# Optimization experiments

Measured on AMD Instinct MI355X. Metric: run time of the kernel, lower is better.

## Reference

```python
import jax, jax.numpy as jnp
import numpy as np

K, PAD, POOL = 3, 1, 2

def _conv_block(x, w, b):
    # x: [B,C,H,W]; w: [O, C*K*K] (Linear weight, feature order (C,kh,kw)); b: [O]
    O = w.shape[0]
    C = x.shape[1]
    ker = w.reshape(O, C, K, K)  # OIHW, matches torch unfold+linear ordering
    y = jax.lax.conv_general_dilated(
        x, ker, window_strides=(1, 1), padding=[(PAD, PAD), (PAD, PAD)],
        dimension_numbers=("NCHW", "OIHW", "NCHW"))
    y = y + b[None, :, None, None]
    y = jax.nn.relu(y)
    # non-overlapping max pool, drops remainder like torch unfold (sizes divisible here)
    y = jax.lax.reduce_window(y, -jnp.inf, jax.lax.max,
                              (1, 1, POOL, POOL), (1, 1, POOL, POOL), "VALID")
    return y

def setup_inputs() -> dict:
    key = jax.random.key(0)
    ks = jax.random.split(key, 9)
    B, Cin, H = 64, 3, 128
    C1, C2, FC, NCLS = 64, 128, 256, 1000
    flat = C2 * (H // 4) * (H // 4)  # 128*32*32 = 131072
    s = 0.05
    return {
        "x": jax.random.normal(ks[0], (B, Cin, H, H), jnp.float32),
        "conv1_w": jax.random.normal(ks[1], (C1, Cin * K * K), jnp.float32) * s,
        "conv1_b": jax.random.normal(ks[2], (C1,), jnp.float32) * s,
        "conv2_w": jax.random.normal(ks[3], (C2, C1 * K * K), jnp.float32) * s,
        "conv2_b": jax.random.normal(ks[4], (C2,), jnp.float32) * s,
        "fc1_w": jax.random.normal(ks[5], (FC, flat), jnp.float32) * 0.005,
        "fc1_b": jax.random.normal(ks[6], (FC,), jnp.float32) * s,
        "fc2_w": jax.random.normal(ks[7], (NCLS, FC), jnp.float32) * s,
        "fc2_b": jax.random.normal(ks[8], (NCLS,), jnp.float32) * s,
    }

def reference(x, conv1_w, conv1_b, conv2_w, conv2_b, fc1_w, fc1_b, fc2_w, fc2_b):
    h = _conv_block(x, conv1_w, conv1_b)      # [B,64,64,64]
    h = _conv_block(h, conv2_w, conv2_b)      # [B,128,32,32]
    h = h.reshape(h.shape[0], -1)             # NCHW flatten, same as torch .view
    h = jax.nn.relu(h @ fc1_w.T + fc1_b)
    return h @ fc2_w.T + fc2_b                # [B,1000]
```

## Files before the change

kernel.cpp:

```cpp
#include <hip/hip_runtime.h>
#include <hip/hip_bf16.h>

typedef __attribute__((ext_vector_type(8))) short short8;
typedef __attribute__((ext_vector_type(4))) float f32x4;

#define KFC   131072
#define NCLS  1000

__device__ __forceinline__ unsigned short f2bf(float f) {
  union { float f; unsigned u; } v; v.f = f;
  unsigned r = v.u + 0x7FFFu + ((v.u >> 16) & 1u);
  return (unsigned short)(r >> 16);
}

__device__ __forceinline__ unsigned pk2bf(float a, float b) {
  __hip_bfloat162 h = __float22bfloat162_rn(float2{a, b});
  union { __hip_bfloat162 h; unsigned u; } c; c.h = h;
  return c.u;
}

__global__ __launch_bounds__(256) void prep_w1(
    const float* __restrict__ w1, short* __restrict__ Bp1) {
  int i = blockIdx.x * 256 + threadIdx.x;
  int o = i >> 5, k = i & 31;
  Bp1[i] = (k < 27) ? (short)f2bf(w1[o * 27 + k]) : (short)0;
}

__global__ __launch_bounds__(256) void conv1_mfma(
    const float* __restrict__ x, const short* __restrict__ Bp1,
    const float* __restrict__ b1, unsigned short* __restrict__ y) {
  __shared__ unsigned short tile[1152];
  const int t = threadIdx.x;
  const int blk = blockIdx.x;
  const int tx = blk & 7, ty = (blk >> 3) & 7, b = blk >> 6;
  const int w = t >> 6, lane = t & 63;
  const int l15 = lane & 15, lg = lane >> 4;

  const int ih0 = ty * 16 - 1, iw0 = tx * 16 - 1;
  for (int i = t; i < 1152; i += 256) {
    unsigned short v = 0;
    if (i < 1080) {
      int ci = i / 360, rem = i - ci * 360;
      int tr = rem / 20, tc = rem - tr * 20;
      int ih = ih0 + tr, iw = iw0 + tc;
      if (tc < 18 && (unsigned)ih < 128u && (unsigned)iw < 128u)
        v = f2bf(x[(b * 3 + ci) * 16384 + (ih << 7) + iw]);
    }
    tile[i] = v;
  }

  short8 bf[4];
#pragma unroll
  for (int n = 0; n < 4; ++n)
    bf[n] = *(const short8*)(Bp1 + ((n * 16 + l15) << 5) + (lg << 3));

  int soff[8];
#pragma unroll
  for (int j = 0; j < 8; ++j) {
    int k = lg * 8 + j;
    if (k < 27) {
      int ci = k / 9, rem = k - ci * 9;
      int r = rem / 3, s = rem - r * 3;
      soff[j] = ci * 360 + r * 20 + s + l15 + w * 80;
    } else {
      soff[j] = 1080;
    }
  }
  __syncthreads();

  f32x4 acc[4][4];
#pragma unroll
  for (int m = 0; m < 4; ++m)
#pragma unroll
    for (int n = 0; n < 4; ++n) acc[m][n] = (f32x4){0.f, 0.f, 0.f, 0.f};

#pragma unroll
  for (int m = 0; m < 4; ++m) {
    union { short8 s; unsigned short u[8]; } af;
#pragma unroll
    for (int j = 0; j < 8; ++j) af.u[j] = tile[soff[j] + m * 20];
#pragma unroll
    for (int n = 0; n < 4; ++n)
      acc[m][n] = __builtin_amdgcn_mfma_f32_16x16x32_bf16(af.s, bf[n], acc[m][n], 0, 0, 0);
  }

#pragma unroll
  for (int n = 0; n < 4; ++n) {
    const int o = n * 16 + l15;
    const float bias = b1[o];
#pragma unroll
    for (int q = 0; q < 2; ++q) {
      const int pr = ty * 8 + w * 2 + q;
      float v0 = fmaxf(fmaxf(acc[2 * q][n][0], acc[2 * q][n][1]),
                       fmaxf(acc[2 * q + 1][n][0], acc[2 * q + 1][n][1]));
      float v1 = fmaxf(fmaxf(acc[2 * q][n][2], acc[2 * q][n][3]),
                       fmaxf(acc[2 * q + 1][n][2], acc[2 * q + 1][n][3]));
      v0 = fmaxf(v0 + bias, 0.f);
      v1 = fmaxf(v1 + bias, 0.f);
      const int pc = tx * 8 + lg * 2;
      unsigned short* dst = y + ((((size_t)b << 6) + pr) << 12) + ((size_t)pc << 6) + o;
      dst[0]  = f2bf(v0);
      dst[64] = f2bf(v1);
    }
  }
}

__global__ __launch_bounds__(256) void prep_w2(
    const float* __restrict__ w2, short* __restrict__ Bp) {
  int i = blockIdx.x * 256 + threadIdx.x;
  int c = i & 31, o = (i >> 5) & 127, pp = i >> 12;
  int cg = pp / 9, pos = pp - cg * 9;
  Bp[i] = (short)f2bf(w2[o * 576 + (cg * 32 + c) * 9 + pos]);
}

__global__ __launch_bounds__(256) void conv2_mfma(
    const short* __restrict__ yin, const short* __restrict__ Bp,
    const float* __restrict__ b2, unsigned int* __restrict__ A32) {
  __shared__ short tile[180 * 36];
  const int t = threadIdx.x;
  const int blk = blockIdx.x;
  const int tx = blk & 3, ty = (blk >> 2) & 7, b = blk >> 5;
  const int w = t >> 6, lane = t & 63;
  const int l15 = lane & 15, lg = lane >> 4;

  f32x4 acc[8][2];
#pragma unroll
  for (int m = 0; m < 8; ++m)
#pragma unroll
    for (int n = 0; n < 2; ++n) acc[m][n] = (f32x4){0.f, 0.f, 0.f, 0.f};

  const int ih0 = ty * 8 - 1, iw0 = tx * 16 - 1;
  const int abase = l15 * 36 + lg * 8;

#pragma unroll
  for (int cg = 0; cg < 2; ++cg) {
    __syncthreads();
    for (int i = t; i < 180 * 4; i += 256) {
      int p = i >> 2, q = i & 3;
      int sy = p / 18, sx = p - sy * 18;
      int ih = ih0 + sy, iw = iw0 + sx;
      short8 v = (short8){0, 0, 0, 0, 0, 0, 0, 0};
      if (((unsigned)ih < 64u) && ((unsigned)iw < 64u))
        v = *(const short8*)(yin + ((((size_t)b << 6) + ih) << 12) + ((size_t)iw << 6) + cg * 32 + q * 8);
      *(short8*)&tile[p * 36 + q * 8] = v;
    }
    __syncthreads();

    short8 afb[2][4];
    short8 bfb[2][2];

#pragma unroll
    for (int n = 0; n < 2; ++n)
      bfb[0][n] = *(const short8*)(Bp + ((((cg * 9 + 0) << 7) + (w * 2 + n) * 16 + l15) << 5) + (lg << 3));
#pragma unroll
    for (int m = 0; m < 4; ++m)
      afb[0][m] = *(const short8*)&tile[m * 648 + abase];

#pragma unroll
    for (int s = 0; s < 18; ++s) {
      const int pos = s >> 1, half = s & 1;
      if (s < 17) {
        const int ns = s + 1, npos = ns >> 1, nhalf = ns & 1;
        if (nhalf == 0) {
#pragma unroll
          for (int n = 0; n < 2; ++n)
            bfb[npos & 1][n] = *(const short8*)(Bp + ((((cg * 9 + npos) << 7) + (w * 2 + n) * 16 + l15) << 5) + (lg << 3));
        }
        const int nkh = npos / 3, nkw = npos - nkh * 3;
#pragma unroll
        for (int m = 0; m < 4; ++m)
          afb[ns & 1][m] = *(const short8*)&tile[(nhalf * 4 + m + nkh) * 648 + nkw * 36 + abase];
      }
#pragma unroll
      for (int n = 0; n < 2; ++n)
#pragma unroll
        for (int m = 0; m < 4; ++m)
          acc[half * 4 + m][n] = __builtin_amdgcn_mfma_f32_16x16x32_bf16(
              afb[s & 1][m], bfb[pos & 1][n], acc[half * 4 + m][n], 0, 0, 0);
    }
  }

  const size_t bbase = ((size_t)b << 16);
#pragma unroll
  for (int n = 0; n < 2; ++n) {
    const int o = (w * 2 + n) * 16 + l15;
    const float bias = b2[o];
#pragma unroll
    for (int mp = 0; mp < 4; ++mp) {
      const int prow = ty * 4 + mp;
      float v0 = fmaxf(fmaxf(acc[2 * mp][n][0], acc[2 * mp][n][1]),
                       fmaxf(acc[2 * mp + 1][n][0], acc[2 * mp + 1][n][1]));
      float v1 = fmaxf(fmaxf(acc[2 * mp][n][2], acc[2 * mp][n][3]),
                       fmaxf(acc[2 * mp + 1][n][2], acc[2 * mp + 1][n][3]));
      v0 = fmaxf(v0 + bias, 0.f);
      v1 = fmaxf(v1 + bias, 0.f);
      unsigned pk = (unsigned)f2bf(v0) | ((unsigned)f2bf(v1) << 16);
      A32[bbase + (size_t)o * 512 + prow * 16 + tx * 4 + lg] = pk;
    }
  }
}

__global__ __launch_bounds__(256) void fc1_mfma(
    const unsigned short* __restrict__ A, const float* __restrict__ W,
    float* __restrict__ P) {
  __shared__ short Al[64][520];
  const int t = threadIdx.x;
  const int blk = blockIdx.x;
  const int kc = blk >> 1, nt = blk & 1;
  const int wn = t >> 6, lane = t & 63;
  const int l15 = lane & 15, lg = lane >> 4;

  {
    const int row = t >> 2, q = t & 3;
    const unsigned short* asrc = A + (size_t)row * KFC + kc * 512 + q * 128;
    short8 ar[16];
#pragma unroll
    for (int i = 0; i < 16; ++i) ar[i] = *(const short8*)(asrc + i * 8);
#pragma unroll
    for (int i = 0; i < 16; ++i) *(short8*)&Al[row][q * 128 + i * 8] = ar[i];
  }
  __syncthreads();

  f32x4 acc[4][2];
#pragma unroll
  for (int m = 0; m < 4; ++m)
#pragma unroll
    for (int n = 0; n < 2; ++n) acc[m][n] = (f32x4){0.f, 0.f, 0.f, 0.f};

  const float* wrow[2];
#pragma unroll
  for (int n = 0; n < 2; ++n)
    wrow[n] = W + (size_t)(nt * 128 + wn * 32 + n * 16 + l15) * KFC + kc * 512 + lg * 8;

#pragma unroll
  for (int ks = 0; ks < 16; ++ks) {
    short8 bf[2];
#pragma unroll
    for (int n = 0; n < 2; ++n) {
      f32x4 u = *(const f32x4*)(wrow[n] + ks * 32);
      f32x4 v = *(const f32x4*)(wrow[n] + ks * 32 + 4);
      union { short8 s; unsigned u32[4]; } pk;
      pk.u32[0] = pk2bf(u[0], u[1]);
      pk.u32[1] = pk2bf(u[2], u[3]);
      pk.u32[2] = pk2bf(v[0], v[1]);
      pk.u32[3] = pk2bf(v[2], v[3]);
      bf[n] = pk.s;
    }
    short8 af[4];
#pragma unroll
    for (int m = 0; m < 4; ++m)
      af[m] = *(const short8*)&Al[m * 16 + l15][ks * 32 + lg * 8];
#pragma unroll
    for (int n = 0; n < 2; ++n)
#pragma unroll
      for (int m = 0; m < 4; ++m)
        acc[m][n] = __builtin_amdgcn_mfma_f32_16x16x32_bf16(af[m], bf[n], acc[m][n], 0, 0, 0);
  }

  float* dst = P + (size_t)kc * 16384;
#pragma unroll
  for (int m = 0; m < 4; ++m)
#pragma unroll
    for (int n = 0; n < 2; ++n)
#pragma unroll
      for (int j = 0; j < 4; ++j) {
        int brow = m * 16 + lg * 4 + j;
        int o = nt * 128 + wn * 32 + n * 16 + l15;
        dst[brow * 256 + o] = acc[m][n][j];
      }
}

__global__ __launch_bounds__(256) void fc1_reduce_kernel(
    const float* __restrict__ P, const float* __restrict__ fb1,
    float* __restrict__ Y) {
  __shared__ float red[4][64];
  const int t = threadIdx.x;
  const int iq = t & 63, pg = t >> 6;
  const int gidx = blockIdx.x * 64 + iq;
  const float* p0 = P + (size_t)(pg * 64) * 16384 + gidx;
  float s0 = 0, s1 = 0, s2 = 0, s3 = 0;
  for (int p = 0; p < 64; p += 4) {
    s0 += p0[(size_t)(p + 0) * 16384];
    s1 += p0[(size_t)(p + 1) * 16384];
    s2 += p0[(size_t)(p + 2) * 16384];
    s3 += p0[(size_t)(p + 3) * 16384];
  }
  red[pg][iq] = (s0 + s1) + (s2 + s3);
  __syncthreads();
  if (pg == 0) {
    float tot = (red[0][iq] + red[1][iq]) + (red[2][iq] + red[3][iq]);
    Y[gidx] = fmaxf(tot + fb1[gidx & 255], 0.f);
  }
}

__global__ __launch_bounds__(256) void fc2_kernel(
    const float* __restrict__ Y, const float* __restrict__ W2,
    const float* __restrict__ b2, float* __restrict__ out) {
  int tid = blockIdx.x * 256 + threadIdx.x;
  if (tid >= 64 * NCLS) return;
  int b = tid / NCLS, n = tid - b * NCLS;
  const float4* yv = (const float4*)(Y + b * 256);
  const float4* wv = (const float4*)(W2 + n * 256);
  float acc = 0.f;
#pragma unroll 8
  for (int f = 0; f < 64; ++f) {
    float4 a = yv[f], w = wv[f];
    acc += a.x * w.x + a.y * w.y + a.z * w.z + a.w * w.w;
  }
  out[tid] = acc + b2[n];
}

extern "C" void kernel_launch(void* const* d_in, const int* in_sizes, int n_in,
                              void* d_out, int out_size, void* d_ws, size_t ws_size,
                              hipStream_t stream) {
  const float* x   = (const float*)d_in[0];
  const float* w1  = (const float*)d_in[1];
  const float* b1  = (const float*)d_in[2];
  const float* w2  = (const float*)d_in[3];
  const float* b2  = (const float*)d_in[4];
  const float* fw1 = (const float*)d_in[5];
  const float* fb1 = (const float*)d_in[6];
  const float* fw2 = (const float*)d_in[7];
  const float* fb2 = (const float*)d_in[8];
  float* out = (float*)d_out;

  unsigned short* Y1 = (unsigned short*)d_ws;
  unsigned short* A16 = Y1 + 16777216;
  short* Bp = (short*)(A16 + 8388608);
  short* Bp1 = Bp + 73728;
  float* P  = (float*)(Bp1 + 2048);
  float* Yf = P + 4194304;

  prep_w2<<<288, 256, 0, stream>>>(w2, Bp);
  prep_w1<<<8, 256, 0, stream>>>(w1, Bp1);
  conv1_mfma<<<4096, 256, 0, stream>>>(x, Bp1, b1, Y1);
  conv2_mfma<<<2048, 256, 0, stream>>>((const short*)Y1, Bp, b2, (unsigned int*)A16);
  fc1_mfma<<<512, 256, 0, stream>>>(A16, fw1, P);
  fc1_reduce_kernel<<<256, 256, 0, stream>>>(P, fb1, Yf);
  fc2_kernel<<<250, 256, 0, stream>>>(Yf, fw2, fb2, out);
}
```

Measured before the change: 116.5 us.

## Switch conv2 to 32x32x16 MFMA with full-channel LDS tile

Conv2 now uses 32x32x16 bf16 MFMA instructions instead of 16x16x32. Each wave computes 32 output channels across 4 pairs of output rows. The LDS tile holds all 64 input channels, so it is loaded once with a single barrier instead of twice. The weight prep kernel is rewritten to match the new 16-channel K-chunk layout. This cuts barriers and LDS reloads and improves operand reuse, at the cost of a larger LDS footprint and possible bank conflicts from the 72-short row stride.

```diff
diff --git a/kernel.cpp b/kernel.cpp
--- a/kernel.cpp
+++ b/kernel.cpp
@@ -3,6 +3,7 @@
 
 typedef __attribute__((ext_vector_type(8))) short short8;
 typedef __attribute__((ext_vector_type(4))) float f32x4;
+typedef __attribute__((ext_vector_type(16))) float f32x16;
 
 #define KFC   131072
 #define NCLS  1000
@@ -108,95 +109,85 @@
 __global__ __launch_bounds__(256) void prep_w2(
     const float* __restrict__ w2, short* __restrict__ Bp) {
   int i = blockIdx.x * 256 + threadIdx.x;
-  int c = i & 31, o = (i >> 5) & 127, pp = i >> 12;
-  int cg = pp / 9, pos = pp - cg * 9;
-  Bp[i] = (short)f2bf(w2[o * 576 + (cg * 32 + c) * 9 + pos]);
+  int c = i & 15, o = (i >> 4) & 127, q = i >> 11;
+  int pos = q >> 2, c4 = q & 3;
+  int ch = c4 * 16 + c;
+  Bp[i] = (short)f2bf(w2[o * 576 + ch * 9 + pos]);
 }
 
 __global__ __launch_bounds__(256) void conv2_mfma(
     const short* __restrict__ yin, const short* __restrict__ Bp,
     const float* __restrict__ b2, unsigned int* __restrict__ A32) {
-  __shared__ short tile[180 * 36];
+  __shared__ short tile[180 * 72];
   const int t = threadIdx.x;
   const int blk = blockIdx.x;
   const int tx = blk & 3, ty = (blk >> 2) & 7, b = blk >> 5;
   const int w = t >> 6, lane = t & 63;
-  const int l15 = lane & 15, lg = lane >> 4;
-
-  f32x4 acc[8][2];
-#pragma unroll
-  for (int m = 0; m < 8; ++m)
-#pragma unroll
-    for (int n = 0; n < 2; ++n) acc[m][n] = (f32x4){0.f, 0.f, 0.f, 0.f};
+  const int l31 = lane & 31, h = lane >> 5;
 
   const int ih0 = ty * 8 - 1, iw0 = tx * 16 - 1;
-  const int abase = l15 * 36 + lg * 8;
-
-#pragma unroll
-  for (int cg = 0; cg < 2; ++cg) {
-    __syncthreads();
-    for (int i = t; i < 180 * 4; i += 256) {
-      int p = i >> 2, q = i & 3;
-      int sy = p / 18, sx = p - sy * 18;
-      int ih = ih0 + sy, iw = iw0 + sx;
-      short8 v = (short8){0, 0, 0, 0, 0, 0, 0, 0};
-      if (((unsigned)ih < 64u) && ((unsigned)iw < 64u))
-        v = *(const short8*)(yin + ((((size_t)b << 6) + ih) << 12) + ((size_t)iw << 6) + cg * 32 + q * 8);
-      *(short8*)&tile[p * 36 + q * 8] = v;
-    }
-    __syncthreads();
-
-    short8 afb[2][4];
-    short8 bfb[2][2];
-
-#pragma unroll
-    for (int n = 0; n < 2; ++n)
-      bfb[0][n] = *(const short8*)(Bp + ((((cg * 9 + 0) << 7) + (w * 2 + n) * 16 + l15) << 5) + (lg << 3));
-#pragma unroll
-    for (int m = 0; m < 4; ++m)
-      afb[0][m] = *(const short8*)&tile[m * 648 + abase];
-
-#pragma unroll
-    for (int s = 0; s < 18; ++s) {
-      const int pos = s >> 1, half = s & 1;
-      if (s < 17) {
-        const int ns = s + 1, npos = ns >> 1, nhalf = ns & 1;
-        if (nhalf == 0) {
-#pragma unroll
-          for (int n = 0; n < 2; ++n)
-            bfb[npos & 1][n] = *(const short8*)(Bp + ((((cg * 9 + npos) << 7) + (w * 2 + n) * 16 + l15) << 5) + (lg << 3));
-        }
-        const int nkh = npos / 3, nkw = npos - nkh * 3;
-#pragma unroll
-        for (int m = 0; m < 4; ++m)
-          afb[ns & 1][m] = *(const short8*)&tile[(nhalf * 4 + m + nkh) * 648 + nkw * 36 + abase];
-      }
-#pragma unroll
-      for (int n = 0; n < 2; ++n)
-#pragma unroll
-        for (int m = 0; m < 4; ++m)
-          acc[half * 4 + m][n] = __builtin_amdgcn_mfma_f32_16x16x32_bf16(
-              afb[s & 1][m], bfb[pos & 1][n], acc[half * 4 + m][n], 0, 0, 0);
-    }
+
+  for (int i = t; i < 1440; i += 256) {
+    int p = i >> 3, q8 = i & 7;
+    int sy = p / 18, sx = p - sy * 18;
+    int ih = ih0 + sy, iw = iw0 + sx;
+    short8 v = (short8){0, 0, 0, 0, 0, 0, 0, 0};
+    if (((unsigned)ih < 64u) && ((unsigned)iw < 64u))
+      v = *(const short8*)(yin + ((((size_t)b << 6) + ih) << 12) + ((size_t)iw << 6) + q8 * 8);
+    *(short8*)&tile[p * 72 + q8 * 8] = v;
+  }
+  __syncthreads();
+
+  f32x16 acc[4];
+#pragma unroll
+  for (int s = 0; s < 4; ++s)
+#pragma unroll
+    for (int j = 0; j < 16; ++j) acc[s][j] = 0.f;
+
+  const int arow = l31 >> 4;
+  const int acol = l31 & 15;
+  const int chof = h * 8;
+  const int obase = w * 32 + l31;
+
+  short8 afb[2][4];
+  short8 bfb[2];
+
+#pragma unroll
+  for (int s = 0; s < 4; ++s)
+    afb[0][s] = *(const short8*)&tile[((2 * s + arow) * 18 + acol) * 72 + chof];
+  bfb[0] = *(const short8*)(Bp + (size_t)obase * 16 + chof);
+
+#pragma unroll
+  for (int q = 0; q < 36; ++q) {
+    if (q < 35) {
+      const int nq = q + 1, npos = nq >> 2, nc4 = nq & 3;
+      const int nkh = npos / 3, nkw = npos - nkh * 3;
+#pragma unroll
+      for (int s = 0; s < 4; ++s)
+        afb[nq & 1][s] = *(const short8*)&tile[((2 * s + arow + nkh) * 18 + acol + nkw) * 72 + nc4 * 16 + chof];
+      bfb[nq & 1] = *(const short8*)(Bp + (size_t)(nq * 128 + obase) * 16 + chof);
+    }
+#pragma unroll
+    for (int s = 0; s < 4; ++s)
+      acc[s] = __builtin_amdgcn_mfma_f32_32x32x16_bf16(afb[q & 1][s], bfb[q & 1], acc[s], 0, 0, 0);
   }
 
   const size_t bbase = ((size_t)b << 16);
-#pragma unroll
-  for (int n = 0; n < 2; ++n) {
-    const int o = (w * 2 + n) * 16 + l15;
-    const float bias = b2[o];
-#pragma unroll
-    for (int mp = 0; mp < 4; ++mp) {
-      const int prow = ty * 4 + mp;
-      float v0 = fmaxf(fmaxf(acc[2 * mp][n][0], acc[2 * mp][n][1]),
-                       fmaxf(acc[2 * mp + 1][n][0], acc[2 * mp + 1][n][1]));
-      float v1 = fmaxf(fmaxf(acc[2 * mp][n][2], acc[2 * mp][n][3]),
-                       fmaxf(acc[2 * mp + 1][n][2], acc[2 * mp + 1][n][3]));
-      v0 = fmaxf(v0 + bias, 0.f);
-      v1 = fmaxf(v1 + bias, 0.f);
-      unsigned pk = (unsigned)f2bf(v0) | ((unsigned)f2bf(v1) << 16);
-      A32[bbase + (size_t)o * 512 + prow * 16 + tx * 4 + lg] = pk;
-    }
+  const float bias = b2[obase];
+#pragma unroll
+  for (int s = 0; s < 4; ++s) {
+    const int prow = ty * 4 + s;
+    float v0 = fmaxf(fmaxf(acc[s][0], acc[s][1]), fmaxf(acc[s][8],  acc[s][9]));
+    float v1 = fmaxf(fmaxf(acc[s][2], acc[s][3]), fmaxf(acc[s][10], acc[s][11]));
+    float v2 = fmaxf(fmaxf(acc[s][4], acc[s][5]), fmaxf(acc[s][12], acc[s][13]));
+    float v3 = fmaxf(fmaxf(acc[s][6], acc[s][7]), fmaxf(acc[s][14], acc[s][15]));
+    v0 = fmaxf(v0 + bias, 0.f);
+    v1 = fmaxf(v1 + bias, 0.f);
+    v2 = fmaxf(v2 + bias, 0.f);
+    v3 = fmaxf(v3 + bias, 0.f);
+    unsigned int* dst = A32 + bbase + (size_t)obase * 512 + prow * 16 + tx * 4 + h;
+    dst[0] = (unsigned)f2bf(v0) | ((unsigned)f2bf(v1) << 16);
+    dst[2] = (unsigned)f2bf(v2) | ((unsigned)f2bf(v3) << 16);
   }
 }
 
```

Result: no change. 117.0 us (+0.4%).
